# Kernel optimization log

Measured on AMD Instinct MI355X. Metric: run time of the kernel, lower is better.

Reference implementation:

```python
import jax, jax.numpy as jnp
import numpy as np

def binarize(t):
    # deterministic sign binarization to {-1, +1}
    return jnp.where(t >= 0, 1.0, -1.0).astype(t.dtype)

def setup_inputs() -> dict:
    key = jax.random.key(0)
    k1, k2 = jax.random.split(key)
    x = jax.random.normal(k1, (8192, 4096), dtype=jnp.float32)
    kernel = jax.random.normal(k2, (4096, 4096), dtype=jnp.float32)
    return {"x": x, "kernel": kernel}

def reference(x, kernel):
    # BinaryLayer.call with binary=True: matmul(binarize(x), binarize(W))
    return jnp.matmul(binarize(x), binarize(kernel))
```

## Files before the change

kernel.cpp:

```cpp
#include <hip/hip_runtime.h>
#include <stdint.h>

#define MDIM 8192
#define NDIM 4096
#define KDIM 4096
#define KB2  (KDIM / 2)
#define BKB  128
#define NKT  (KDIM / 256)

#define BM 256
#define BN 256
#define ABUF      32768
#define BUFSTRIDE 65536

typedef __attribute__((ext_vector_type(4))) int   i32x4;
typedef __attribute__((ext_vector_type(8))) int   i32x8;
typedef __attribute__((ext_vector_type(4))) float f32x4;

__device__ __forceinline__ void gload16(const void* g, void* l) {
    __builtin_amdgcn_global_load_lds(
        (const __attribute__((address_space(1))) void*)g,
        (__attribute__((address_space(3))) void*)l, 16, 0, 0);
}

__device__ __forceinline__ i32x8 pad8(i32x4 v) {
    i32x8 r;
    r[0] = v[0]; r[1] = v[1]; r[2] = v[2]; r[3] = v[3];
    r[4] = 0;    r[5] = 0;    r[6] = 0;    r[7] = 0;
    return r;
}

#define MFMA_FP4(a, b, c)                                                   \
    __builtin_amdgcn_mfma_scale_f32_16x16x128_f8f6f4(                        \
        (a), (b), (c), 4, 4, 0, 0x7F7F7F7F, 0, 0x7F7F7F7F)

__global__ __launch_bounds__(256) void pack_a4_kernel(const float* __restrict__ X,
                                                      uint8_t* __restrict__ A4) {
    size_t gt = (size_t)blockIdx.x * 256 + threadIdx.x;
    const float4* x4 = (const float4*)X + gt * 4;
    uint32_t out[2] = {0, 0};
#pragma unroll
    for (int q = 0; q < 4; ++q) {
        float4 v = x4[q];
        uint32_t b0 = (v.x >= 0.f ? 0x2u : 0xAu) | ((v.y >= 0.f ? 0x2u : 0xAu) << 4);
        uint32_t b1 = (v.z >= 0.f ? 0x2u : 0xAu) | ((v.w >= 0.f ? 0x2u : 0xAu) << 4);
        out[q >> 1] |= (b0 | (b1 << 8)) << ((q & 1) * 16);
    }
    ((uint2*)A4)[gt] = make_uint2(out[0], out[1]);
}

__global__ __launch_bounds__(256) void pack_b4t_kernel(const float* __restrict__ W,
                                                       uint8_t* __restrict__ B4) {
    __shared__ uint8_t t[64][72];
    const int tid = threadIdx.x;
    const int k0 = blockIdx.y * 64, n0 = blockIdx.x * 64;
#pragma unroll
    for (int r = 0; r < 4; ++r) {
        int e  = r * 1024 + tid * 4;
        int k  = e >> 6;
        int nn = e & 63;
        float4 v = *(const float4*)&W[(size_t)(k0 + k) * NDIM + n0 + nn];
        uint32_t b0 = (v.x >= 0.f) ? 0x2u : 0xAu;
        uint32_t b1 = (v.y >= 0.f) ? 0x2u : 0xAu;
        uint32_t b2 = (v.z >= 0.f) ? 0x2u : 0xAu;
        uint32_t b3 = (v.w >= 0.f) ? 0x2u : 0xAu;
        *(uint32_t*)&t[k][nn] = b0 | (b1 << 8) | (b2 << 16) | (b3 << 24);
    }
    __syncthreads();
    const int n = tid >> 2, kc = tid & 3;
    uint32_t w[2] = {0, 0};
#pragma unroll
    for (int b = 0; b < 8; ++b) {
        int k = kc * 16 + b * 2;
        uint32_t byte = (uint32_t)t[k][n] | ((uint32_t)t[k + 1][n] << 4);
        w[b >> 2] |= byte << ((b & 3) * 8);
    }
    *(uint2*)&B4[(size_t)(n0 + n) * KB2 + k0 / 2 + kc * 8] = make_uint2(w[0], w[1]);
}

__global__ __launch_bounds__(512, 2) void binmm_fp4_kernel(const uint8_t* __restrict__ A4,
                                                           const uint8_t* __restrict__ B4,
                                                           float* __restrict__ C) {
    __shared__ uint8_t lds[2 * BUFSTRIDE];

    const int tid = threadIdx.x, lane = tid & 63, wid = tid >> 6;
    const int wr = wid >> 2, wc = wid & 3;
    const int l15 = lane & 15, g = (lane >> 4) & 3;
    const int m0 = blockIdx.y * BM, n0 = blockIdx.x * BN;

    const int srow  = tid >> 3;
    const int sslot = tid & 7;
    const uint8_t* gA[4];
    const uint8_t* gB[4];
#pragma unroll
    for (int p = 0; p < 4; ++p) {
        int row = srow + p * 64;
        int ss  = (sslot ^ (row & 7)) * 16;
        gA[p] = A4 + (size_t)(m0 + row) * KB2 + ss;
        gB[p] = B4 + (size_t)(n0 + row) * KB2 + ss;
    }

    f32x4 acc[8][4];
#pragma unroll
    for (int m = 0; m < 8; ++m)
#pragma unroll
        for (int n = 0; n < 4; ++n) acc[m][n] = (f32x4){0.f, 0.f, 0.f, 0.f};

#pragma unroll
    for (int p = 0; p < 4; ++p) {
        gload16(gA[p], lds + tid * 16 + p * 8192);
        gload16(gB[p], lds + ABUF + tid * 16 + p * 8192);
        gA[p] += BKB;
        gB[p] += BKB;
    }
    __syncthreads();

    int cur = 0;
    for (int t = 0; t < NKT; ++t) {
        if (t + 1 < NKT) {
            uint8_t* nb = lds + (cur ^ 1) * BUFSTRIDE;
#pragma unroll
            for (int p = 0; p < 4; ++p) {
                gload16(gA[p], nb + tid * 16 + p * 8192);
                gload16(gB[p], nb + ABUF + tid * 16 + p * 8192);
                gA[p] += BKB;
                gB[p] += BKB;
            }
        }

        const uint8_t* Acur = lds + cur * BUFSTRIDE;
        const uint8_t* Bcur = Acur + ABUF;
#pragma unroll
        for (int s = 0; s < 2; ++s) {
            i32x8 bf[4];
#pragma unroll
            for (int n = 0; n < 4; ++n) {
                int row  = wc * 64 + n * 16 + l15;
                int slot = ((s * 4 + g) ^ (row & 7)) * 16;
                bf[n] = pad8(*(const i32x4*)(Bcur + row * 128 + slot));
            }
            __builtin_amdgcn_s_setprio(1);
#pragma unroll
            for (int m = 0; m < 8; ++m) {
                int row  = wr * 128 + m * 16 + l15;
                int slot = ((s * 4 + g) ^ (row & 7)) * 16;
                i32x8 af = pad8(*(const i32x4*)(Acur + row * 128 + slot));
                acc[m][0] = MFMA_FP4(af, bf[0], acc[m][0]);
                acc[m][1] = MFMA_FP4(af, bf[1], acc[m][1]);
                acc[m][2] = MFMA_FP4(af, bf[2], acc[m][2]);
                acc[m][3] = MFMA_FP4(af, bf[3], acc[m][3]);
            }
            __builtin_amdgcn_s_setprio(0);
        }

        __syncthreads();
        cur ^= 1;
    }

#pragma unroll
    for (int m = 0; m < 8; ++m) {
#pragma unroll
        for (int n = 0; n < 4; ++n) {
            size_t cc = (size_t)(n0 + wc * 64 + n * 16 + l15);
            int rbase = m0 + wr * 128 + m * 16 + g * 4;
#pragma unroll
            for (int reg = 0; reg < 4; ++reg)
                C[(size_t)(rbase + reg) * NDIM + cc] = acc[m][n][reg];
        }
    }
}

extern "C" void kernel_launch(void* const* d_in, const int* in_sizes, int n_in,
                              void* d_out, int out_size, void* d_ws, size_t ws_size,
                              hipStream_t stream) {
    const float* x = (const float*)d_in[0];
    const float* w = (const float*)d_in[1];
    float* out = (float*)d_out;

    uint8_t* A4 = (uint8_t*)d_ws;
    uint8_t* B4 = (uint8_t*)d_ws + (size_t)MDIM * KB2;

    pack_a4_kernel<<<(int)((size_t)MDIM * KDIM / 16 / 256), 256, 0, stream>>>(x, A4);
    pack_b4t_kernel<<<dim3(NDIM / 64, KDIM / 64), 256, 0, stream>>>(w, B4);
    binmm_fp4_kernel<<<dim3(NDIM / BN, MDIM / BM), 512, 0, stream>>>(A4, B4, out);
}
```

Baseline: 124.8 us.

## Switch FP4 GEMM to 32x32x64 MFMA with interleaved LDS reads and staging

Replaces the 16x16x128 scaled FP4 MFMA with the 32x32x64 variant, so each wave computes a 4x2 grid of 32x32 tiles and needs fewer LDS fragment reads per unit of compute. The main loop is also restructured: the tile loop is unrolled by two with fixed buffer offsets, and global-to-LDS staging of A and B is interleaved with double-buffered register fragment reads and MFMA clusters. The aim is to cut LDS traffic and overlap memory with compute. In exchange, register pressure rises and the output store layout changes to match the 32x32 accumulator mapping.

After: 122.8 us. About the same (-1.6%).

```diff
diff --git a/kernel.cpp b/kernel.cpp
--- a/kernel.cpp
+++ b/kernel.cpp
@@ -13,9 +13,9 @@
 #define ABUF      32768
 #define BUFSTRIDE 65536
 
-typedef __attribute__((ext_vector_type(4))) int   i32x4;
-typedef __attribute__((ext_vector_type(8))) int   i32x8;
-typedef __attribute__((ext_vector_type(4))) float f32x4;
+typedef __attribute__((ext_vector_type(4)))  int   i32x4;
+typedef __attribute__((ext_vector_type(8)))  int   i32x8;
+typedef __attribute__((ext_vector_type(16))) float f32x16;
 
 __device__ __forceinline__ void gload16(const void* g, void* l) {
     __builtin_amdgcn_global_load_lds(
@@ -30,8 +30,8 @@
     return r;
 }
 
-#define MFMA_FP4(a, b, c)                                                   \
-    __builtin_amdgcn_mfma_scale_f32_16x16x128_f8f6f4(                        \
+#define MFMA_FP4_32(a, b, c)                                                 \
+    __builtin_amdgcn_mfma_scale_f32_32x32x64_f8f6f4(                          \
         (a), (b), (c), 4, 4, 0, 0x7F7F7F7F, 0, 0x7F7F7F7F)
 
 __global__ __launch_bounds__(256) void pack_a4_kernel(const float* __restrict__ X,
@@ -85,7 +85,7 @@
 
     const int tid = threadIdx.x, lane = tid & 63, wid = tid >> 6;
     const int wr = wid >> 2, wc = wid & 3;
-    const int l15 = lane & 15, g = (lane >> 4) & 3;
+    const int l31 = lane & 31, kh = lane >> 5;
     const int m0 = blockIdx.y * BM, n0 = blockIdx.x * BN;
 
     const int srow  = tid >> 3;
@@ -100,72 +100,93 @@
         gB[p] = B4 + (size_t)(n0 + row) * KB2 + ss;
     }
 
-    f32x4 acc[8][4];
-#pragma unroll
-    for (int m = 0; m < 8; ++m)
-#pragma unroll
-        for (int n = 0; n < 4; ++n) acc[m][n] = (f32x4){0.f, 0.f, 0.f, 0.f};
-
-#pragma unroll
-    for (int p = 0; p < 4; ++p) {
-        gload16(gA[p], lds + tid * 16 + p * 8192);
-        gload16(gB[p], lds + ABUF + tid * 16 + p * 8192);
-        gA[p] += BKB;
-        gB[p] += BKB;
-    }
+    f32x16 acc[4][2];
+#pragma unroll
+    for (int m = 0; m < 4; ++m)
+#pragma unroll
+        for (int n = 0; n < 2; ++n)
+#pragma unroll
+            for (int e = 0; e < 16; ++e) acc[m][n][e] = 0.f;
+
+    auto stageA = [&](int nxt) {
+#pragma unroll
+        for (int p = 0; p < 4; ++p) {
+            gload16(gA[p], lds + nxt + tid * 16 + p * 8192);
+            gA[p] += BKB;
+        }
+    };
+    auto stageB = [&](int nxt) {
+#pragma unroll
+        for (int p = 0; p < 4; ++p) {
+            gload16(gB[p], lds + nxt + ABUF + tid * 16 + p * 8192);
+            gB[p] += BKB;
+        }
+    };
+
+#define RDA(dst, cur, s) do {                                                  \
+        _Pragma("unroll")                                                      \
+        for (int mf = 0; mf < 4; ++mf) {                                       \
+            int row = wr * 128 + mf * 32 + l31;                                \
+            dst[mf] = *(const i32x4*)(lds + (cur) + row * 128 +                \
+                                      ((((s) * 2 + kh) ^ (row & 7)) * 16));    \
+        }                                                                      \
+    } while (0)
+#define RDB(dst, cur, s) do {                                                  \
+        _Pragma("unroll")                                                      \
+        for (int nf = 0; nf < 2; ++nf) {                                       \
+            int row = wc * 64 + nf * 32 + l31;                                 \
+            dst[nf] = *(const i32x4*)(lds + (cur) + ABUF + row * 128 +         \
+                                      ((((s) * 2 + kh) ^ (row & 7)) * 16));    \
+        }                                                                      \
+    } while (0)
+#define CLUSTER(AS, BS) do {                                                   \
+        __builtin_amdgcn_s_setprio(1);                                         \
+        _Pragma("unroll")                                                      \
+        for (int mf = 0; mf < 4; ++mf) {                                       \
+            i32x8 a8 = pad8(AS[mf]);                                           \
+            acc[mf][0] = MFMA_FP4_32(a8, pad8(BS[0]), acc[mf][0]);             \
+            acc[mf][1] = MFMA_FP4_32(a8, pad8(BS[1]), acc[mf][1]);             \
+        }                                                                      \
+        __builtin_amdgcn_s_setprio(0);                                         \
+    } while (0)
+
+    auto tile = [&](int cur, int nxt, bool do_stage) {
+        i32x4 aP[4], bP[2], aQ[4], bQ[2];
+        RDA(aP, cur, 0); RDB(bP, cur, 0);
+        if (do_stage) stageA(nxt);
+        RDA(aQ, cur, 1); RDB(bQ, cur, 1);
+        CLUSTER(aP, bP);
+        if (do_stage) stageB(nxt);
+        RDA(aP, cur, 2); RDB(bP, cur, 2);
+        CLUSTER(aQ, bQ);
+        RDA(aQ, cur, 3); RDB(bQ, cur, 3);
+        CLUSTER(aP, bP);
+        CLUSTER(aQ, bQ);
+        __syncthreads();
+    };
+
+    stageA(0); stageB(0);
     __syncthreads();
 
-    int cur = 0;
-    for (int t = 0; t < NKT; ++t) {
-        if (t + 1 < NKT) {
-            uint8_t* nb = lds + (cur ^ 1) * BUFSTRIDE;
-#pragma unroll
-            for (int p = 0; p < 4; ++p) {
-                gload16(gA[p], nb + tid * 16 + p * 8192);
-                gload16(gB[p], nb + ABUF + tid * 16 + p * 8192);
-                gA[p] += BKB;
-                gB[p] += BKB;
+#pragma unroll 1
+    for (int tt = 0; tt < NKT / 2 - 1; ++tt) {
+        tile(0, BUFSTRIDE, true);
+        tile(BUFSTRIDE, 0, true);
+    }
+    tile(0, BUFSTRIDE, true);
+    tile(BUFSTRIDE, 0, false);
+
+#pragma unroll
+    for (int mf = 0; mf < 4; ++mf) {
+#pragma unroll
+        for (int nf = 0; nf < 2; ++nf) {
+            size_t cc = (size_t)(n0 + wc * 64 + nf * 32 + l31);
+            int rbase = m0 + wr * 128 + mf * 32 + 4 * kh;
+#pragma unroll
+            for (int reg = 0; reg < 16; ++reg) {
+                int rr = (reg & 3) + 8 * (reg >> 2);
+                C[(size_t)(rbase + rr) * NDIM + cc] = acc[mf][nf][reg];
             }
-        }
-
-        const uint8_t* Acur = lds + cur * BUFSTRIDE;
-        const uint8_t* Bcur = Acur + ABUF;
-#pragma unroll
-        for (int s = 0; s < 2; ++s) {
-            i32x8 bf[4];
-#pragma unroll
-            for (int n = 0; n < 4; ++n) {
-                int row  = wc * 64 + n * 16 + l15;
-                int slot = ((s * 4 + g) ^ (row & 7)) * 16;
-                bf[n] = pad8(*(const i32x4*)(Bcur + row * 128 + slot));
-            }
-            __builtin_amdgcn_s_setprio(1);
-#pragma unroll
-            for (int m = 0; m < 8; ++m) {
-                int row  = wr * 128 + m * 16 + l15;
-                int slot = ((s * 4 + g) ^ (row & 7)) * 16;
-                i32x8 af = pad8(*(const i32x4*)(Acur + row * 128 + slot));
-                acc[m][0] = MFMA_FP4(af, bf[0], acc[m][0]);
-                acc[m][1] = MFMA_FP4(af, bf[1], acc[m][1]);
-                acc[m][2] = MFMA_FP4(af, bf[2], acc[m][2]);
-                acc[m][3] = MFMA_FP4(af, bf[3], acc[m][3]);
-            }
-            __builtin_amdgcn_s_setprio(0);
-        }
-
-        __syncthreads();
-        cur ^= 1;
-    }
-
-#pragma unroll
-    for (int m = 0; m < 8; ++m) {
-#pragma unroll
-        for (int n = 0; n < 4; ++n) {
-            size_t cc = (size_t)(n0 + wc * 64 + n * 16 + l15);
-            int rbase = m0 + wr * 128 + m * 16 + g * 4;
-#pragma unroll
-            for (int reg = 0; reg < 4; ++reg)
-                C[(size_t)(rbase + reg) * NDIM + cc] = acc[m][n][reg];
         }
     }
 }
```
